# Kernel optimization log

Measured on AMD Instinct MI355X. Metric: run time of the kernel, lower is better.

Reference implementation:

```python
import jax, jax.numpy as jnp
import numpy as np

EPS = 1e-8
NEG = -1e9


def setup_inputs() -> dict:
    key = jax.random.key(0)
    k = jax.random.split(key, 5)
    B, C, T, D = 32, 512, 2000, 128
    return {
        "x": jax.random.normal(k[0], (B, C, T), dtype=jnp.float32),
        "attn_w": jax.random.normal(k[1], (D, 3 * C), dtype=jnp.float32) * 0.02,
        "attn_b": jax.random.normal(k[2], (D,), dtype=jnp.float32) * 0.02,
        "ctx_w": jax.random.normal(k[3], (C, D), dtype=jnp.float32) * 0.02,
        "ctx_b": jax.random.normal(k[4], (C,), dtype=jnp.float32) * 0.02,
        "mask": jnp.ones((B, T), dtype=jnp.int32),
    }


def reference(x, attn_w, attn_b, ctx_w, ctx_b, mask):
    # x: (B, C, T); mask: (B, T) with 1 = valid frame
    m = mask.astype(x.dtype)[:, None, :]                      # (B, 1, T)
    lengths = jnp.sum(m, axis=2, keepdims=True)               # (B, 1, 1)
    mean = jnp.sum(x * m, axis=2, keepdims=True) / lengths    # (B, C, 1)
    var = jnp.sum(jnp.square(x - mean) * m, axis=2, keepdims=True) / lengths
    std = jnp.sqrt(jnp.clip(var, EPS))                        # (B, C, 1)
    # global context: concat [x, mean, std] along channels -> (B, 3C, T)
    T = x.shape[2]
    context = jnp.concatenate(
        [x, jnp.broadcast_to(mean, x.shape), jnp.broadcast_to(std, x.shape)], axis=1
    )
    # two 1x1 convs == channel GEMMs
    alpha = jnp.tanh(jnp.einsum("dc,bct->bdt", attn_w, context) + attn_b[None, :, None])
    alpha = jnp.einsum("cd,bdt->bct", ctx_w, alpha) + ctx_b[None, :, None]  # (B, C, T)
    alpha = jnp.where(m == 0, NEG, alpha)
    alpha = jax.nn.softmax(alpha, axis=2)
    pooled_mean = jnp.sum(alpha * x, axis=2)                  # (B, C)
    pooled_var = jnp.sum(alpha * jnp.square(x - pooled_mean[:, :, None]), axis=2)
    pooled_std = jnp.sqrt(jnp.clip(pooled_var, EPS))
    return jnp.concatenate([pooled_mean, pooled_std], axis=1)  # (B, 2C)
```

## Files before the change

### kernel.cpp

```cpp
#include <hip/hip_runtime.h>
#include <hip/hip_bf16.h>
#include <math.h>

#define EPSF 1e-8f
typedef __attribute__((ext_vector_type(8))) short short8;
typedef __attribute__((ext_vector_type(4))) short s4v;
typedef __attribute__((ext_vector_type(4))) float f32x4;

__device__ __forceinline__ float wred_sum(float v) {
#pragma unroll
  for (int o = 32; o > 0; o >>= 1) v += __shfl_down(v, o, 64);
  return v;
}

static __device__ __forceinline__ unsigned short f2bf(float f) {
  __hip_bfloat16 h = __float2bfloat16(f);
  return *reinterpret_cast<unsigned short*>(&h);
}
static __device__ __forceinline__ float bf2f(unsigned short u) {
  unsigned int v = ((unsigned int)u) << 16;
  float f;
  __builtin_memcpy(&f, &v, 4);
  return f;
}

__global__ __launch_bounds__(256) void k_zc(
    const float* __restrict__ attn_w, const float* __restrict__ ctx_w,
    const int* __restrict__ mask, unsigned short* __restrict__ awb,
    unsigned short* __restrict__ cwb, float* __restrict__ zp,
    float* __restrict__ Lbuf, int nz4, int C, int D, int B, int T) {
  int i = blockIdx.x * 256 + threadIdx.x;
  int DC = D * C;
  if (i < DC) {
    int d = i / C, c = i % C;
    awb[i] = f2bf(attn_w[(size_t)d * 3 * C + c]);
  } else if (i < 2 * DC) {
    int j = i - DC;
    cwb[j] = f2bf(ctx_w[j]);
  }
  if (i < nz4)
    *reinterpret_cast<float4*>(zp + (size_t)i * 4) = (float4){0.f, 0.f, 0.f, 0.f};
  if (blockIdx.x < B) {
    int b = blockIdx.x;
    const int* mr = mask + (size_t)b * T;
    float sl = 0.f;
    for (int t = threadIdx.x; t < T; t += 256) sl += (float)mr[t];
    __shared__ float rl[4];
    sl = wred_sum(sl);
    if ((threadIdx.x & 63) == 0) rl[threadIdx.x >> 6] = sl;
    __syncthreads();
    if (threadIdx.x == 0) Lbuf[b] = rl[0] + rl[1] + rl[2] + rl[3];
  }
}

__global__ __launch_bounds__(256) void k_ms_tr(
    const float* __restrict__ x, const int* __restrict__ mask,
    float* __restrict__ sums, unsigned short* __restrict__ xbT, int C, int T) {
  int b = blockIdx.z, c0 = blockIdx.x * 64, tbase = blockIdx.y * 256;
  int tid = threadIdx.x;
  int row = tid >> 2, q = tid & 3;
  __shared__ unsigned short Xb[64][72];
  const float* xr = x + ((size_t)b * C + c0 + row) * T;
  const int* mr = mask + (size_t)b * T;
  float s1 = 0.f, s2 = 0.f;

  int rem = T - tbase;
  int ntt = rem >= 256 ? 4 : (rem + 63) >> 6;

  float4 rx[4];
  int4 rm[4];

#define LOADT(st)                                                              \
  {                                                                            \
    int t0_ = tbase + (st) * 64;                                               \
    _Pragma("unroll")                                                          \
    for (int ss = 0; ss < 4; ss++) {                                           \
      int t = t0_ + (q + 4 * ss) * 4;                                          \
      if (t + 3 < T) {                                                         \
        rx[ss] = *reinterpret_cast<const float4*>(&xr[t]);                     \
        rm[ss] = *reinterpret_cast<const int4*>(&mr[t]);                       \
      } else {                                                                 \
        rx[ss].x = (t < T) ? xr[t] : 0.f;     rm[ss].x = (t < T) ? mr[t] : 0;  \
        rx[ss].y = (t+1 < T) ? xr[t+1] : 0.f; rm[ss].y = (t+1 < T) ? mr[t+1] : 0;\
        rx[ss].z = (t+2 < T) ? xr[t+2] : 0.f; rm[ss].z = (t+2 < T) ? mr[t+2] : 0;\
        rx[ss].w = (t+3 < T) ? xr[t+3] : 0.f; rm[ss].w = (t+3 < T) ? mr[t+3] : 0;\
      }                                                                        \
    }                                                                          \
  }

  LOADT(0);

#pragma unroll
  for (int tt = 0; tt < 4; tt++) {
    if (tt >= ntt) break;
    int t0 = tbase + tt * 64;
#pragma unroll
    for (int ss = 0; ss < 4; ss++) {
      float4 v = rx[ss];
      float m0 = (float)rm[ss].x, m1 = (float)rm[ss].y;
      float m2 = (float)rm[ss].z, m3 = (float)rm[ss].w;
      s1 += m0 * v.x + m1 * v.y + m2 * v.z + m3 * v.w;
      s2 += m0 * v.x * v.x + m1 * v.y * v.y + m2 * v.z * v.z + m3 * v.w * v.w;
      int tl = (q + 4 * ss) * 4;
      Xb[tl + 0][row] = f2bf(v.x);
      Xb[tl + 1][row] = f2bf(v.y);
      Xb[tl + 2][row] = f2bf(v.z);
      Xb[tl + 3][row] = f2bf(v.w);
    }
    if (tt + 1 < ntt) LOADT(tt + 1);
    __syncthreads();
    {
      int trow = tid >> 2;
      int t = t0 + trow;
      if (t < T) {
        unsigned short* dst = &xbT[((size_t)b * T + t) * C + c0 + q * 16];
        *reinterpret_cast<short8*>(dst) =
            *reinterpret_cast<const short8*>(&Xb[trow][q * 16]);
        *reinterpret_cast<short8*>(dst + 8) =
            *reinterpret_cast<const short8*>(&Xb[trow][q * 16 + 8]);
      }
    }
    if (tt + 1 < ntt) __syncthreads();
  }
#undef LOADT

  s1 += __shfl_down(s1, 2, 4); s1 += __shfl_down(s1, 1, 4);
  s2 += __shfl_down(s2, 2, 4); s2 += __shfl_down(s2, 1, 4);
  if (q == 0) {
    float* sp = &sums[((size_t)b * C + c0 + row) * 2];
    atomicAdd(sp, s1);
    atomicAdd(sp + 1, s2);
  }
}

__global__ __launch_bounds__(256) void k_bias2f(
    const float* __restrict__ attn_w, const float* __restrict__ attn_b,
    const float* __restrict__ sums, const float* __restrict__ Lbuf,
    float* __restrict__ bias2, int C, int D) {
  int nb = D >> 2;
  int b = blockIdx.x / nb;
  int d = (blockIdx.x % nb) * 4 + (threadIdx.x >> 6);
  int lane = threadIdx.x & 63;
  float L = fmaxf(Lbuf[b], 1.f);
  const float* wr = attn_w + (size_t)d * 3 * C;
  float s = 0.f;
  for (int c = lane; c < C; c += 64) {
    float s1 = sums[((size_t)b * C + c) * 2];
    float s2 = sums[((size_t)b * C + c) * 2 + 1];
    float mu = s1 / L;
    float var = s2 / L - mu * mu;
    float sd = sqrtf(fmaxf(var, EPSF));
    s += wr[C + c] * mu + wr[2 * C + c] * sd;
  }
  s = wred_sum(s);
  if (lane == 0) bias2[(size_t)b * D + d] = attn_b[d] + s;
}

__global__ __launch_bounds__(256) void k_gemm1(
    const unsigned short* __restrict__ xbT, const unsigned short* __restrict__ awb,
    const float* __restrict__ bias2, unsigned short* __restrict__ alphaT,
    int C, int T, int D) {
  int b = blockIdx.y;
  int t0 = blockIdx.x * 64;
  int tid = threadIdx.x;
  int w = tid >> 6, lane = tid & 63;
  int l15 = lane & 15, g = lane >> 4;
  __shared__ unsigned short As[64][72];
  __shared__ unsigned short Bs[128][72];
  f32x4 acc[4][2];
#pragma unroll
  for (int i = 0; i < 4; i++)
#pragma unroll
    for (int j = 0; j < 2; j++) acc[i][j] = (f32x4){0.f, 0.f, 0.f, 0.f};

  int ar = tid >> 2, aq = tid & 3;
  int dr = tid >> 1, h = tid & 1;
  bool okA = (t0 + ar) < T;
  size_t rowA = ((size_t)b * T + t0 + ar) * C + aq * 16;
  size_t rowB = (size_t)dr * C + h * 32;

  short8 ra[2], rb[4];
  ra[0] = okA ? *reinterpret_cast<const short8*>(&xbT[rowA]) : (short8){};
  ra[1] = okA ? *reinterpret_cast<const short8*>(&xbT[rowA + 8]) : (short8){};
#pragma unroll
  for (int qq = 0; qq < 4; qq++)
    rb[qq] = *reinterpret_cast<const short8*>(&awb[rowB + qq * 8]);

  for (int c0 = 0; c0 < C; c0 += 64) {
    __syncthreads();
    *reinterpret_cast<short8*>(&As[ar][aq * 16]) = ra[0];
    *reinterpret_cast<short8*>(&As[ar][aq * 16 + 8]) = ra[1];
#pragma unroll
    for (int qq = 0; qq < 4; qq++)
      *reinterpret_cast<short8*>(&Bs[dr][h * 32 + qq * 8]) = rb[qq];
    if (c0 + 64 < C) {
      size_t nA = rowA + c0 + 64, nB = rowB + c0 + 64;
      ra[0] = okA ? *reinterpret_cast<const short8*>(&xbT[nA]) : (short8){};
      ra[1] = okA ? *reinterpret_cast<const short8*>(&xbT[nA + 8]) : (short8){};
#pragma unroll
      for (int qq = 0; qq < 4; qq++)
        rb[qq] = *reinterpret_cast<const short8*>(&awb[nB + qq * 8]);
    }
    __syncthreads();
#pragma unroll
    for (int ks = 0; ks < 2; ks++) {
      short8 a[4], bb[2];
#pragma unroll
      for (int tf = 0; tf < 4; tf++)
        a[tf] = *reinterpret_cast<const short8*>(&As[tf * 16 + l15][ks * 32 + g * 8]);
#pragma unroll
      for (int df = 0; df < 2; df++)
        bb[df] = *reinterpret_cast<const short8*>(&Bs[w * 32 + df * 16 + l15][ks * 32 + g * 8]);
#pragma unroll
      for (int tf = 0; tf < 4; tf++)
#pragma unroll
        for (int df = 0; df < 2; df++)
          acc[tf][df] = __builtin_amdgcn_mfma_f32_16x16x32_bf16(a[tf], bb[df], acc[tf][df], 0, 0, 0);
    }
  }
#pragma unroll
  for (int df = 0; df < 2; df++) {
    int d = w * 32 + df * 16 + l15;
    float bias = bias2[(size_t)b * D + d];
#pragma unroll
    for (int tf = 0; tf < 4; tf++)
#pragma unroll
      for (int r = 0; r < 4; r++) {
        int t = t0 + tf * 16 + g * 4 + r;
        if (t < T)
          alphaT[((size_t)b * T + t) * D + d] = f2bf(tanhf(bias + acc[tf][df][r]));
      }
  }
}

__global__ __launch_bounds__(256) void k_pool2(
    const unsigned short* __restrict__ alphaT, const unsigned short* __restrict__ cwb,
    const unsigned short* __restrict__ xbT, const int* __restrict__ mask,
    float* __restrict__ Sacc, int C, int T, int D) {
  int b = blockIdx.z;
  int c0 = blockIdx.y * 64;
  int ch0 = blockIdx.x * 512;
  int tid = threadIdx.x;
  int w = tid >> 6, lane = tid & 63, l15 = lane & 15, g = lane >> 4;
  __shared__ unsigned short Bl[2][64][136];

  short8 a[4];
#pragma unroll
  for (int ks = 0; ks < 4; ks++)
    a[ks] = *reinterpret_cast<const short8*>(
        &cwb[(size_t)(c0 + w * 16 + l15) * D + ks * 32 + g * 8]);
  int cbase = c0 + w * 16 + g * 4;
  float S0[4] = {0.f, 0.f, 0.f, 0.f};
  float S1[4] = {0.f, 0.f, 0.f, 0.f};
  float S2[4] = {0.f, 0.f, 0.f, 0.f};

  const int* mr = mask + (size_t)b * T;
  int srow = tid >> 2, sq = tid & 3;

  int rem = T - ch0;
  int ntt = rem >= 512 ? 8 : (rem + 63) >> 6;

  short8 pa0, pa1, pa2, pa3;
  s4v xv[2][4];
  const unsigned short* xbb = &xbT[(size_t)b * T * C];

#define LOADSUB(st)                                                            \
  {                                                                            \
    int trow = ch0 + (st) * 64 + srow;                                         \
    pa0 = pa1 = pa2 = pa3 = (short8){};                                        \
    if (trow < T) {                                                            \
      const unsigned short* sa = &alphaT[((size_t)b * T + trow) * D + sq * 32];\
      pa0 = *reinterpret_cast<const short8*>(sa);                              \
      pa1 = *reinterpret_cast<const short8*>(sa + 8);                          \
      pa2 = *reinterpret_cast<const short8*>(sa + 16);                         \
      pa3 = *reinterpret_cast<const short8*>(sa + 24);                         \
    }                                                                          \
  }

#define WRITESUB(bufi)                                                         \
  {                                                                            \
    *reinterpret_cast<short8*>(&Bl[bufi][srow][sq * 32]) = pa0;                \
    *reinterpret_cast<short8*>(&Bl[bufi][srow][sq * 32 + 8]) = pa1;            \
    *reinterpret_cast<short8*>(&Bl[bufi][srow][sq * 32 + 16]) = pa2;           \
    *reinterpret_cast<short8*>(&Bl[bufi][srow][sq * 32 + 24]) = pa3;           \
  }

#define GXV(pi, st)                                                            \
  {                                                                            \
    _Pragma("unroll")                                                          \
    for (int tf_ = 0; tf_ < 4; tf_++) {                                        \
      int t_ = ch0 + (st) * 64 + tf_ * 16 + l15;                               \
      int tc_ = t_ < T ? t_ : T - 1;                                           \
      xv[pi][tf_] = *reinterpret_cast<const s4v*>(&xbb[(size_t)tc_ * C + cbase]);\
    }                                                                          \
  }

  LOADSUB(0);
  WRITESUB(0);
  if (ntt > 1) LOADSUB(1);
  GXV(0, 0);
  if (ntt > 1) GXV(1, 1);
  __syncthreads();

#pragma unroll
  for (int k = 0; k < 8; k++) {
    if (k >= ntt) break;
    int buf = k & 1;
    if (k + 1 < ntt) {
      WRITESUB((k + 1) & 1);
      if (k + 2 < ntt) LOADSUB(k + 2);
    }
    int t0 = ch0 + k * 64;
#pragma unroll
    for (int tf = 0; tf < 4; tf++) {
      f32x4 p = (f32x4){0.f, 0.f, 0.f, 0.f};
#pragma unroll
      for (int ks = 0; ks < 4; ks++) {
        short8 bb = *reinterpret_cast<const short8*>(
            &Bl[buf][tf * 16 + l15][ks * 32 + g * 8]);
        p = __builtin_amdgcn_mfma_f32_16x16x32_bf16(a[ks], bb, p, 0, 0, 0);
      }
      int t = t0 + tf * 16 + l15;
      bool valid = (t < T) && (mr[t < T ? t : 0] != 0);
#pragma unroll
      for (int r = 0; r < 4; r++) {
        float e = valid ? __expf(p[r]) : 0.f;
        float xvf = bf2f((unsigned short)xv[buf][tf][r]);
        S0[r] += e; S1[r] += e * xvf; S2[r] += e * xvf * xvf;
      }
    }
    if (k + 2 < ntt) GXV(buf, k + 2);
    __syncthreads();
  }
#undef LOADSUB
#undef WRITESUB
#undef GXV

#pragma unroll
  for (int r = 0; r < 4; r++) {
#pragma unroll
    for (int o = 1; o < 16; o <<= 1) {
      S0[r] += __shfl_xor(S0[r], o, 16);
      S1[r] += __shfl_xor(S1[r], o, 16);
      S2[r] += __shfl_xor(S2[r], o, 16);
    }
  }
  if (l15 == 0) {
#pragma unroll
    for (int r = 0; r < 4; r++) {
      float* sp = &Sacc[((size_t)b * C + cbase + r) * 3];
      atomicAdd(sp, S0[r]);
      atomicAdd(sp + 1, S1[r]);
      atomicAdd(sp + 2, S2[r]);
    }
  }
}

__global__ __launch_bounds__(256) void k_out(
    const float* __restrict__ Sacc, float* __restrict__ out, int C) {
  int b = blockIdx.x;
  for (int c = threadIdx.x; c < C; c += 256) {
    float S0 = Sacc[((size_t)b * C + c) * 3];
    float S1 = Sacc[((size_t)b * C + c) * 3 + 1];
    float S2 = Sacc[((size_t)b * C + c) * 3 + 2];
    float pm = S1 / S0;
    float var = S2 / S0 - pm * pm;
    out[(size_t)b * 2 * C + c] = pm;
    out[(size_t)b * 2 * C + C + c] = sqrtf(fmaxf(var, EPSF));
  }
}

extern "C" void kernel_launch(void* const* d_in, const int* in_sizes, int n_in,
                              void* d_out, int out_size, void* d_ws, size_t ws_size,
                              hipStream_t stream) {
  const float* x = (const float*)d_in[0];
  const float* attn_w = (const float*)d_in[1];
  const float* attn_b = (const float*)d_in[2];
  const float* ctx_w = (const float*)d_in[3];
  const int* mask = (const int*)d_in[5];
  float* out = (float*)d_out;

  int D = in_sizes[2];
  int C = in_sizes[4];
  int B = out_size / (2 * C);
  int T = in_sizes[5] / B;

  unsigned short* awb = (unsigned short*)d_ws;
  unsigned short* cwb = awb + (size_t)D * C;
  float* bias2 = (float*)(cwb + (size_t)C * D);
  float* Lbuf = bias2 + (size_t)B * D;
  float* sums = Lbuf + B;
  float* Sacc = sums + (size_t)B * C * 2;
  unsigned short* xbT = (unsigned short*)(Sacc + (size_t)B * C * 3);
  unsigned short* alphaT = xbT + (size_t)B * T * C;

  int nz4 = (B * C * 5 + 3) / 4;
  int zcn = 2 * D * C;
  if (nz4 > zcn) zcn = nz4;
  k_zc<<<(zcn + 255) / 256, 256, 0, stream>>>(
      attn_w, ctx_w, mask, awb, cwb, sums, Lbuf, nz4, C, D, B, T);
  k_ms_tr<<<dim3(C / 64, (T + 255) / 256, B), 256, 0, stream>>>(x, mask, sums, xbT, C, T);
  k_bias2f<<<B * (D / 4), 256, 0, stream>>>(attn_w, attn_b, sums, Lbuf, bias2, C, D);
  k_gemm1<<<dim3((T + 63) / 64, B), 256, 0, stream>>>(xbT, awb, bias2, alphaT, C, T, D);
  k_pool2<<<dim3((T + 511) / 512, C / 64, B), 256, 0, stream>>>(
      alphaT, cwb, xbT, mask, Sacc, C, T, D);
  k_out<<<B, 256, 0, stream>>>(Sacc, out, C);
}
```

Baseline: 117.2 us.

## Fuse mean/std stats and bf16 transpose into first GEMM, defer tanh

Merges the statistics/transpose pass with the first channel GEMM so x is read once, converted to bf16 in shared memory, and consumed directly by MFMA while also writing xbT and accumulating sums. Since the mean/std bias depends on completed sums, the bias add and tanh move into a separate elementwise kernel over alphaT. This removes the GEMM's re-read of xbT but adds an extra pass over alphaT, stores the pre-activation in bf16 before the bias (a small precision change), and gives fewer blocks in the fused kernel.

```diff
diff --git a/kernel.cpp b/kernel.cpp
--- a/kernel.cpp
+++ b/kernel.cpp
@@ -53,83 +53,138 @@
   }
 }
 
-__global__ __launch_bounds__(256) void k_ms_tr(
+__global__ __launch_bounds__(256) void k_fwd1(
     const float* __restrict__ x, const int* __restrict__ mask,
-    float* __restrict__ sums, unsigned short* __restrict__ xbT, int C, int T) {
-  int b = blockIdx.z, c0 = blockIdx.x * 64, tbase = blockIdx.y * 256;
+    const unsigned short* __restrict__ awb, float* __restrict__ sums,
+    unsigned short* __restrict__ xbT, unsigned short* __restrict__ alphaT,
+    int C, int T, int D) {
+  int b = blockIdx.y;
+  int t0 = blockIdx.x * 64;
   int tid = threadIdx.x;
-  int row = tid >> 2, q = tid & 3;
-  __shared__ unsigned short Xb[64][72];
-  const float* xr = x + ((size_t)b * C + c0 + row) * T;
+  int w = tid >> 6, lane = tid & 63;
+  int l15 = lane & 15, g = lane >> 4;
+  __shared__ unsigned short As[64][72];
+  __shared__ unsigned short Bs[128][72];
+
+  int cr = tid >> 2, q = tid & 3;
+  int dr = tid >> 1, h = tid & 1;
+
   const int* mr = mask + (size_t)b * T;
-  float s1 = 0.f, s2 = 0.f;
-
-  int rem = T - tbase;
-  int ntt = rem >= 256 ? 4 : (rem + 63) >> 6;
+  float mv[16];
+#pragma unroll
+  for (int ss = 0; ss < 4; ss++)
+#pragma unroll
+    for (int j = 0; j < 4; j++) {
+      int t = t0 + (q + 4 * ss) * 4 + j;
+      mv[ss * 4 + j] = (t < T && mr[t] != 0) ? 1.f : 0.f;
+    }
+
+  f32x4 acc[4][2];
+#pragma unroll
+  for (int i = 0; i < 4; i++)
+#pragma unroll
+    for (int j = 0; j < 2; j++) acc[i][j] = (f32x4){0.f, 0.f, 0.f, 0.f};
 
   float4 rx[4];
-  int4 rm[4];
-
-#define LOADT(st)                                                              \
+  short8 rb[4];
+
+#define LOADX(cc0)                                                             \
   {                                                                            \
-    int t0_ = tbase + (st) * 64;                                               \
+    const float* xr_ = x + ((size_t)b * C + (cc0) + cr) * T;                   \
     _Pragma("unroll")                                                          \
     for (int ss = 0; ss < 4; ss++) {                                           \
-      int t = t0_ + (q + 4 * ss) * 4;                                          \
+      int t = t0 + (q + 4 * ss) * 4;                                           \
       if (t + 3 < T) {                                                         \
-        rx[ss] = *reinterpret_cast<const float4*>(&xr[t]);                     \
-        rm[ss] = *reinterpret_cast<const int4*>(&mr[t]);                       \
+        rx[ss] = *reinterpret_cast<const float4*>(&xr_[t]);                    \
       } else {                                                                 \
-        rx[ss].x = (t < T) ? xr[t] : 0.f;     rm[ss].x = (t < T) ? mr[t] : 0;  \
-        rx[ss].y = (t+1 < T) ? xr[t+1] : 0.f; rm[ss].y = (t+1 < T) ? mr[t+1] : 0;\
-        rx[ss].z = (t+2 < T) ? xr[t+2] : 0.f; rm[ss].z = (t+2 < T) ? mr[t+2] : 0;\
-        rx[ss].w = (t+3 < T) ? xr[t+3] : 0.f; rm[ss].w = (t+3 < T) ? mr[t+3] : 0;\
+        rx[ss].x = (t < T) ? xr_[t] : 0.f;                                     \
+        rx[ss].y = (t + 1 < T) ? xr_[t + 1] : 0.f;                             \
+        rx[ss].z = (t + 2 < T) ? xr_[t + 2] : 0.f;                             \
+        rx[ss].w = (t + 3 < T) ? xr_[t + 3] : 0.f;                             \
       }                                                                        \
     }                                                                          \
   }
 
-  LOADT(0);
-
-#pragma unroll
-  for (int tt = 0; tt < 4; tt++) {
-    if (tt >= ntt) break;
-    int t0 = tbase + tt * 64;
+#define LOADB(cc0)                                                             \
+  {                                                                            \
+    size_t base_ = (size_t)dr * C + (cc0) + h * 32;                            \
+    _Pragma("unroll")                                                          \
+    for (int qq = 0; qq < 4; qq++)                                             \
+      rb[qq] = *reinterpret_cast<const short8*>(&awb[base_ + qq * 8]);         \
+  }
+
+  LOADX(0);
+  LOADB(0);
+
+  for (int c0 = 0; c0 < C; c0 += 64) {
+    __syncthreads();
+    float s1 = 0.f, s2 = 0.f;
 #pragma unroll
     for (int ss = 0; ss < 4; ss++) {
       float4 v = rx[ss];
-      float m0 = (float)rm[ss].x, m1 = (float)rm[ss].y;
-      float m2 = (float)rm[ss].z, m3 = (float)rm[ss].w;
-      s1 += m0 * v.x + m1 * v.y + m2 * v.z + m3 * v.w;
-      s2 += m0 * v.x * v.x + m1 * v.y * v.y + m2 * v.z * v.z + m3 * v.w * v.w;
+      s1 += mv[ss*4+0]*v.x + mv[ss*4+1]*v.y + mv[ss*4+2]*v.z + mv[ss*4+3]*v.w;
+      s2 += mv[ss*4+0]*v.x*v.x + mv[ss*4+1]*v.y*v.y + mv[ss*4+2]*v.z*v.z + mv[ss*4+3]*v.w*v.w;
       int tl = (q + 4 * ss) * 4;
-      Xb[tl + 0][row] = f2bf(v.x);
-      Xb[tl + 1][row] = f2bf(v.y);
-      Xb[tl + 2][row] = f2bf(v.z);
-      Xb[tl + 3][row] = f2bf(v.w);
-    }
-    if (tt + 1 < ntt) LOADT(tt + 1);
+      As[tl + 0][cr] = f2bf(v.x);
+      As[tl + 1][cr] = f2bf(v.y);
+      As[tl + 2][cr] = f2bf(v.z);
+      As[tl + 3][cr] = f2bf(v.w);
+    }
+#pragma unroll
+    for (int qq = 0; qq < 4; qq++)
+      *reinterpret_cast<short8*>(&Bs[dr][h * 32 + qq * 8]) = rb[qq];
+    s1 += __shfl_down(s1, 2, 4); s1 += __shfl_down(s1, 1, 4);
+    s2 += __shfl_down(s2, 2, 4); s2 += __shfl_down(s2, 1, 4);
+    if (q == 0) {
+      float* sp = &sums[((size_t)b * C + c0 + cr) * 2];
+      atomicAdd(sp, s1);
+      atomicAdd(sp + 1, s2);
+    }
+    if (c0 + 64 < C) {
+      LOADX(c0 + 64);
+      LOADB(c0 + 64);
+    }
     __syncthreads();
+#pragma unroll
+    for (int ks = 0; ks < 2; ks++) {
+      short8 a[4], bb[2];
+#pragma unroll
+      for (int tf = 0; tf < 4; tf++)
+        a[tf] = *reinterpret_cast<const short8*>(&As[tf * 16 + l15][ks * 32 + g * 8]);
+#pragma unroll
+      for (int df = 0; df < 2; df++)
+        bb[df] = *reinterpret_cast<const short8*>(&Bs[w * 32 + df * 16 + l15][ks * 32 + g * 8]);
+#pragma unroll
+      for (int tf = 0; tf < 4; tf++)
+#pragma unroll
+        for (int df = 0; df < 2; df++)
+          acc[tf][df] = __builtin_amdgcn_mfma_f32_16x16x32_bf16(a[tf], bb[df], acc[tf][df], 0, 0, 0);
+    }
     {
-      int trow = tid >> 2;
-      int t = t0 + trow;
+      int t = t0 + cr;
       if (t < T) {
         unsigned short* dst = &xbT[((size_t)b * T + t) * C + c0 + q * 16];
         *reinterpret_cast<short8*>(dst) =
-            *reinterpret_cast<const short8*>(&Xb[trow][q * 16]);
+            *reinterpret_cast<const short8*>(&As[cr][q * 16]);
         *reinterpret_cast<short8*>(dst + 8) =
-            *reinterpret_cast<const short8*>(&Xb[trow][q * 16 + 8]);
+            *reinterpret_cast<const short8*>(&As[cr][q * 16 + 8]);
       }
     }
-    if (tt + 1 < ntt) __syncthreads();
-  }
-#undef LOADT
-
-  s1 += __shfl_down(s1, 2, 4); s1 += __shfl_down(s1, 1, 4);
-  s2 += __shfl_down(s2, 2, 4); s2 += __shfl_down(s2, 1, 4);
-  if (q == 0) {
-    float* sp = &sums[((size_t)b * C + c0 + row) * 2];
-    atomicAdd(sp, s1);
-    atomicAdd(sp + 1, s2);
+  }
+#undef LOADX
+#undef LOADB
+
+#pragma unroll
+  for (int df = 0; df < 2; df++) {
+    int d = w * 32 + df * 16 + l15;
+#pragma unroll
+    for (int tf = 0; tf < 4; tf++)
+#pragma unroll
+      for (int r = 0; r < 4; r++) {
+        int t = t0 + tf * 16 + g * 4 + r;
+        if (t < T)
+          alphaT[((size_t)b * T + t) * D + d] = f2bf(acc[tf][df][r]);
+      }
   }
 }
 
@@ -156,81 +211,22 @@
   if (lane == 0) bias2[(size_t)b * D + d] = attn_b[d] + s;
 }
 
-__global__ __launch_bounds__(256) void k_gemm1(
-    const unsigned short* __restrict__ xbT, const unsigned short* __restrict__ awb,
-    const float* __restrict__ bias2, unsigned short* __restrict__ alphaT,
-    int C, int T, int D) {
-  int b = blockIdx.y;
-  int t0 = blockIdx.x * 64;
-  int tid = threadIdx.x;
-  int w = tid >> 6, lane = tid & 63;
-  int l15 = lane & 15, g = lane >> 4;
-  __shared__ unsigned short As[64][72];
-  __shared__ unsigned short Bs[128][72];
-  f32x4 acc[4][2];
-#pragma unroll
-  for (int i = 0; i < 4; i++)
-#pragma unroll
-    for (int j = 0; j < 2; j++) acc[i][j] = (f32x4){0.f, 0.f, 0.f, 0.f};
-
-  int ar = tid >> 2, aq = tid & 3;
-  int dr = tid >> 1, h = tid & 1;
-  bool okA = (t0 + ar) < T;
-  size_t rowA = ((size_t)b * T + t0 + ar) * C + aq * 16;
-  size_t rowB = (size_t)dr * C + h * 32;
-
-  short8 ra[2], rb[4];
-  ra[0] = okA ? *reinterpret_cast<const short8*>(&xbT[rowA]) : (short8){};
-  ra[1] = okA ? *reinterpret_cast<const short8*>(&xbT[rowA + 8]) : (short8){};
-#pragma unroll
-  for (int qq = 0; qq < 4; qq++)
-    rb[qq] = *reinterpret_cast<const short8*>(&awb[rowB + qq * 8]);
-
-  for (int c0 = 0; c0 < C; c0 += 64) {
-    __syncthreads();
-    *reinterpret_cast<short8*>(&As[ar][aq * 16]) = ra[0];
-    *reinterpret_cast<short8*>(&As[ar][aq * 16 + 8]) = ra[1];
-#pragma unroll
-    for (int qq = 0; qq < 4; qq++)
-      *reinterpret_cast<short8*>(&Bs[dr][h * 32 + qq * 8]) = rb[qq];
-    if (c0 + 64 < C) {
-      size_t nA = rowA + c0 + 64, nB = rowB + c0 + 64;
-      ra[0] = okA ? *reinterpret_cast<const short8*>(&xbT[nA]) : (short8){};
-      ra[1] = okA ? *reinterpret_cast<const short8*>(&xbT[nA + 8]) : (short8){};
-#pragma unroll
-      for (int qq = 0; qq < 4; qq++)
-        rb[qq] = *reinterpret_cast<const short8*>(&awb[nB + qq * 8]);
-    }
-    __syncthreads();
-#pragma unroll
-    for (int ks = 0; ks < 2; ks++) {
-      short8 a[4], bb[2];
-#pragma unroll
-      for (int tf = 0; tf < 4; tf++)
-        a[tf] = *reinterpret_cast<const short8*>(&As[tf * 16 + l15][ks * 32 + g * 8]);
-#pragma unroll
-      for (int df = 0; df < 2; df++)
-        bb[df] = *reinterpret_cast<const short8*>(&Bs[w * 32 + df * 16 + l15][ks * 32 + g * 8]);
-#pragma unroll
-      for (int tf = 0; tf < 4; tf++)
-#pragma unroll
-        for (int df = 0; df < 2; df++)
-          acc[tf][df] = __builtin_amdgcn_mfma_f32_16x16x32_bf16(a[tf], bb[df], acc[tf][df], 0, 0, 0);
-    }
-  }
-#pragma unroll
-  for (int df = 0; df < 2; df++) {
-    int d = w * 32 + df * 16 + l15;
-    float bias = bias2[(size_t)b * D + d];
-#pragma unroll
-    for (int tf = 0; tf < 4; tf++)
-#pragma unroll
-      for (int r = 0; r < 4; r++) {
-        int t = t0 + tf * 16 + g * 4 + r;
-        if (t < T)
-          alphaT[((size_t)b * T + t) * D + d] = f2bf(tanhf(bias + acc[tf][df][r]));
-      }
-  }
+__global__ __launch_bounds__(256) void k_tanh(
+    unsigned short* __restrict__ alphaT, const float* __restrict__ bias2,
+    int T, int D, int total8) {
+  int i = blockIdx.x * 256 + threadIdx.x;
+  if (i >= total8) return;
+  size_t base = (size_t)i * 8;
+  int d0 = (int)(base % D);
+  size_t bt = base / D;
+  int b = (int)(bt / T);
+  const float* bp = &bias2[(size_t)b * D + d0];
+  short8 raw = *reinterpret_cast<const short8*>(&alphaT[base]);
+  unsigned short o[8];
+#pragma unroll
+  for (int j = 0; j < 8; j++)
+    o[j] = f2bf(tanhf(bf2f((unsigned short)raw[j]) + bp[j]));
+  *reinterpret_cast<short8*>(&alphaT[base]) = *reinterpret_cast<short8*>(&o[0]);
 }
 
 __global__ __launch_bounds__(256) void k_pool2(
@@ -399,9 +395,11 @@
   if (nz4 > zcn) zcn = nz4;
   k_zc<<<(zcn + 255) / 256, 256, 0, stream>>>(
       attn_w, ctx_w, mask, awb, cwb, sums, Lbuf, nz4, C, D, B, T);
-  k_ms_tr<<<dim3(C / 64, (T + 255) / 256, B), 256, 0, stream>>>(x, mask, sums, xbT, C, T);
+  k_fwd1<<<dim3((T + 63) / 64, B), 256, 0, stream>>>(
+      x, mask, awb, sums, xbT, alphaT, C, T, D);
   k_bias2f<<<B * (D / 4), 256, 0, stream>>>(attn_w, attn_b, sums, Lbuf, bias2, C, D);
-  k_gemm1<<<dim3((T + 63) / 64, B), 256, 0, stream>>>(xbT, awb, bias2, alphaT, C, T, D);
+  int total8 = (int)((size_t)B * T * D / 8);
+  k_tanh<<<(total8 + 255) / 256, 256, 0, stream>>>(alphaT, bias2, T, D, total8);
   k_pool2<<<dim3((T + 511) / 512, C / 64, B), 256, 0, stream>>>(
       alphaT, cwb, xbT, mask, Sacc, C, T, D);
   k_out<<<B, 256, 0, stream>>>(Sacc, out, C);
```

New measurement: 122.6 us. 4.6% more time.
